# Performance work log

Hardware: AMD Instinct MI355X
Metric: run time of the kernel (lower is better)

## Reference

```python
import jax, jax.numpy as jnp
import numpy as np
from jax.scipy.special import logsumexp


def _lstm(x, mask, Wk, Wr, b, reverse=False):
    # x: [B,T,D], mask: [B,T] bool. Keras LSTM defaults: gate order i,f,g,o,
    # sigmoid recurrent activation, tanh activation. Masked steps carry state.
    if reverse:
        x = x[:, ::-1]
        mask = mask[:, ::-1]
    B, T, _ = x.shape
    H = Wr.shape[0]
    xz = jnp.einsum('btd,dh->bth', x, Wk) + b  # [B,T,4H] input projections, done once

    def step(carry, inp):
        h, c = carry
        z_t, m = inp  # [B,4H], [B]
        z = z_t + h @ Wr
        i, f, g, o = jnp.split(z, 4, axis=-1)
        i = jax.nn.sigmoid(i)
        f = jax.nn.sigmoid(f)
        g = jnp.tanh(g)
        o = jax.nn.sigmoid(o)
        c_new = f * c + i * g
        h_new = o * jnp.tanh(c_new)
        m = m[:, None]
        h = jnp.where(m, h_new, h)
        c = jnp.where(m, c_new, c)
        return (h, c), h

    h0 = jnp.zeros((B, H), x.dtype)
    (_, _), hs = jax.lax.scan(step, (h0, h0), (xz.transpose(1, 0, 2), mask.T))
    hs = hs.transpose(1, 0, 2)  # [B,T,H]
    if reverse:
        hs = hs[:, ::-1]
    return hs


def _crf_log_likelihood(logits, tags, lengths, trans):
    # TFA crf_log_likelihood: sequence_score - log_norm (forward algorithm)
    B, T, C = logits.shape
    t_idx = jnp.arange(T)
    mask = t_idx[None, :] < lengths[:, None]  # [B,T]
    # unary score: sum_t logits[b,t,tags[b,t]] over valid t
    unary = jnp.take_along_axis(logits, tags[..., None], axis=2)[..., 0]
    unary = jnp.sum(jnp.where(mask, unary, 0.0), axis=1)
    # binary score: sum_t trans[tags[t], tags[t+1]] for t < len-1
    binary = trans[tags[:, :-1], tags[:, 1:]]  # [B,T-1]
    mask2 = t_idx[None, : T - 1] < (lengths - 1)[:, None]
    binary = jnp.sum(jnp.where(mask2, binary, 0.0), axis=1)
    # log normalizer via forward algorithm scan
    alpha0 = logits[:, 0]  # [B,C]

    def step(alpha, inp):
        logit_t, m = inp  # [B,C], [B]
        new = logsumexp(alpha[:, :, None] + trans[None], axis=1) + logit_t
        alpha = jnp.where(m[:, None], new, alpha)
        return alpha, None

    alpha, _ = jax.lax.scan(step, alpha0,
                            (logits[:, 1:].transpose(1, 0, 2), mask[:, 1:].T))
    log_norm = logsumexp(alpha, axis=1)
    return unary + binary - log_norm


def setup_inputs() -> dict:
    key = jax.random.key(0)
    ks = jax.random.split(key, 12)
    V, D, H, C, B, T = 30000, 300, 256, 9, 64, 512
    lengths = jax.random.randint(ks[0], (B,), T // 4, T + 1).astype(jnp.int32)
    valid = jnp.arange(T)[None, :] < lengths[:, None]
    inputs = (jax.random.randint(ks[1], (B, T), 1, V) * valid).astype(jnp.int32)
    targets = (jax.random.randint(ks[2], (B, T), 0, C) * valid).astype(jnp.int32)
    s = 0.05
    return {
        'inputs': inputs,
        'inputs_length': lengths,
        'targets': targets,
        'embedding': jax.random.normal(ks[3], (V, D), jnp.float32) * s,
        'Wk_f': jax.random.normal(ks[4], (D, 4 * H), jnp.float32) * s,
        'Wr_f': jax.random.normal(ks[5], (H, 4 * H), jnp.float32) * s,
        'b_f': jnp.zeros((4 * H,), jnp.float32),
        'Wk_b': jax.random.normal(ks[6], (D, 4 * H), jnp.float32) * s,
        'Wr_b': jax.random.normal(ks[7], (H, 4 * H), jnp.float32) * s,
        'b_b': jnp.zeros((4 * H,), jnp.float32),
        'dense_W': jax.random.normal(ks[8], (2 * H, C), jnp.float32) * s,
        'dense_b': jnp.zeros((C,), jnp.float32),
        'trans': jax.random.uniform(ks[9], (C, C), jnp.float32),
    }


def reference(inputs, inputs_length, targets, embedding, Wk_f, Wr_f, b_f,
              Wk_b, Wr_b, b_b, dense_W, dense_b, trans):
    T = inputs.shape[1]
    mask = jnp.arange(T)[None, :] < inputs_length[:, None]  # [B,T]
    emb = embedding[inputs]  # [B,T,D] (dropout is identity in inference)
    h_f = _lstm(emb, mask, Wk_f, Wr_f, b_f, reverse=False)
    h_b = _lstm(emb, mask, Wk_b, Wr_b, b_b, reverse=True)
    h = jnp.concatenate([h_f, h_b], axis=-1)  # [B,T,2H]
    logits = h @ dense_W + dense_b  # [B,T,C]
    log_likelihood = _crf_log_likelihood(logits, targets, inputs_length, trans)
    return logits, log_likelihood, trans
```

## Files before the change

kernel.cpp:

```cpp
#include <hip/hip_runtime.h>
#include <cstdint>
#include <cstddef>

typedef unsigned int  u32;
typedef unsigned short u16;
typedef _Float16 f16;
typedef _Float16 f16x2 __attribute__((ext_vector_type(2)));
typedef _Float16 half8 __attribute__((ext_vector_type(8)));
typedef float    f32x4v __attribute__((ext_vector_type(4)));
typedef int      i32x4 __attribute__((ext_vector_type(4)));

#define BATCH 64
#define TSEQ  512
#define DEMB  300
#define KPAD  320
#define HDIM  256
#define G4    1024
#define NCLS  9

__device__ __forceinline__ u32 packf16(float a, float b) {
  f16x2 v; v.x = (f16)a; v.y = (f16)b;
  return __builtin_bit_cast(u32, v);
}
__device__ __forceinline__ float f16f(u16 x) {
  return (float)__builtin_bit_cast(f16, x);
}
__device__ __forceinline__ float sigm_fast(float x) {
  return __builtin_amdgcn_rcpf(1.f + __expf(-x));
}
__device__ __forceinline__ float tanh_fast(float x) {
  float ax = __builtin_fabsf(x);
  float e = __expf(-2.f * ax);
  float t = (1.f - e) * __builtin_amdgcn_rcpf(1.f + e);
  return copysignf(t, x);
}

__global__ __launch_bounds__(256) void embcvt_k(const float* __restrict__ emb,
                                                u16* __restrict__ out) {
  const int v  = blockIdx.x * 16 + (threadIdx.x >> 4);
  const int kc = threadIdx.x & 15;
  u32* __restrict__ dst = (u32*)(out + (size_t)v * KPAD + kc * 20);
  if (kc < 15) {
    const float* __restrict__ src = emb + (size_t)v * DEMB + kc * 20;
    float tmp[20];
#pragma unroll
    for (int j = 0; j < 20; ++j) tmp[j] = src[j];
#pragma unroll
    for (int j = 0; j < 10; ++j) dst[j] = packf16(tmp[2 * j], tmp[2 * j + 1]);
  } else {
#pragma unroll
    for (int j = 0; j < 10; ++j) dst[j] = 0u;
  }
}

__global__ __launch_bounds__(256) void wkt_k(const float* __restrict__ Wk_f,
                                             const float* __restrict__ Wk_b,
                                             u16* __restrict__ wkt) {
  const int dir = blockIdx.y;
  const float* __restrict__ Wk = dir ? Wk_b : Wk_f;
  const int col = blockIdx.x * 16 + (threadIdx.x >> 4);
  const int kc  = threadIdx.x & 15;
  u32* __restrict__ dst = (u32*)(wkt + ((size_t)dir * G4 + col) * KPAD + kc * 20);
  if (kc < 15) {
    float tmp[20];
#pragma unroll
    for (int j = 0; j < 20; ++j) tmp[j] = Wk[(size_t)(kc * 20 + j) * G4 + col];
#pragma unroll
    for (int j = 0; j < 10; ++j) dst[j] = packf16(tmp[2 * j], tmp[2 * j + 1]);
  } else {
#pragma unroll
    for (int j = 0; j < 10; ++j) dst[j] = 0u;
  }
}

__global__ __launch_bounds__(256) void wr8_k(const float* __restrict__ Wr_f,
                                             const float* __restrict__ Wr_b,
                                             signed char* __restrict__ wr8) {
  const int dir = blockIdx.y;
  const float* __restrict__ Wr = dir ? Wr_b : Wr_f;
  const int col = blockIdx.x * 16 + (threadIdx.x >> 4);
  const int k0  = (threadIdx.x & 15) * 16;
  float tmp[16];
#pragma unroll
  for (int j = 0; j < 16; ++j) tmp[j] = Wr[(size_t)(k0 + j) * G4 + col];
  u32 pw[4];
#pragma unroll
  for (int jj = 0; jj < 4; ++jj) {
    u32 p = 0;
#pragma unroll
    for (int b = 0; b < 4; ++b) {
      int q = (int)__builtin_rintf(tmp[4 * jj + b] * 512.f);
      q = q > 127 ? 127 : (q < -127 ? -127 : q);
      p |= ((u32)(q & 255)) << (8 * b);
    }
    pw[jj] = p;
  }
  *(uint4*)(wr8 + ((size_t)dir * G4 + col) * HDIM + k0) =
      make_uint4(pw[0], pw[1], pw[2], pw[3]);
}

__global__ __launch_bounds__(256) void xz_gemm_k(
    const int* __restrict__ inputs, const u16* __restrict__ wkt,
    const u16* __restrict__ embf16, const float* __restrict__ b_f,
    const float* __restrict__ b_b, u16* __restrict__ xz)
{
  __shared__ __align__(16) u16 As[128 * 40];
  __shared__ __align__(16) u16 Bs[128 * 40];
  const int tid  = threadIdx.x;
  const int wv   = tid >> 6, lane = tid & 63;
  const int quad = lane >> 4, fl = lane & 15;
  const int cbi  = blockIdx.x;
  const int dir  = cbi >> 3;
  const int cb1  = (cbi & 7) * 128;
  const int rb   = blockIdx.y * 128;
  const float* __restrict__ bias = dir ? b_b : b_f;

  const int sm = tid >> 1, sh = (tid & 1) * 16;
  const int vrow = inputs[rb + sm];
  const u16* __restrict__ asrc = wkt + ((size_t)(dir * G4) + cb1 + sm) * KPAD + sh;
  const u16* __restrict__ bsrc = embf16 + (size_t)vrow * KPAD + sh;

  f32x4v acc[2][8];
#pragma unroll
  for (int bt = 0; bt < 2; ++bt)
#pragma unroll
    for (int i = 0; i < 8; ++i) acc[bt][i] = (f32x4v){0.f, 0.f, 0.f, 0.f};

  for (int kt = 0; kt < 10; ++kt) {
    const int k0 = kt * 32;
    uint4 a0v = *(const uint4*)(asrc + k0);
    uint4 a1v = *(const uint4*)(asrc + k0 + 8);
    uint4 b0v = *(const uint4*)(bsrc + k0);
    uint4 b1v = *(const uint4*)(bsrc + k0 + 8);
    *(uint4*)&As[sm * 40 + sh]     = a0v;
    *(uint4*)&As[sm * 40 + sh + 8] = a1v;
    *(uint4*)&Bs[sm * 40 + sh]     = b0v;
    *(uint4*)&Bs[sm * 40 + sh + 8] = b1v;
    __syncthreads();
    half8 bf[2];
#pragma unroll
    for (int bt = 0; bt < 2; ++bt)
      bf[bt] = *(const half8*)&Bs[(wv * 32 + bt * 16 + fl) * 40 + quad * 8];
#pragma unroll
    for (int i = 0; i < 8; ++i) {
      half8 af = *(const half8*)&As[(i * 16 + fl) * 40 + quad * 8];
      acc[0][i] = __builtin_amdgcn_mfma_f32_16x16x32_f16(af, bf[0], acc[0][i], 0, 0, 0);
      acc[1][i] = __builtin_amdgcn_mfma_f32_16x16x32_f16(af, bf[1], acc[1][i], 0, 0, 0);
    }
    __syncthreads();
  }
#pragma unroll
  for (int bt = 0; bt < 2; ++bt) {
    const int row = rb + wv * 32 + bt * 16 + fl;
    u16* __restrict__ orow = xz + ((size_t)(dir * BATCH * TSEQ) + row) * G4;
#pragma unroll
    for (int i = 0; i < 8; ++i) {
      const int mb = cb1 + i * 16 + quad * 4;
      const float4 bb = *(const float4*)&bias[mb];
      f32x4v v = acc[bt][i];
      uint2 pk;
      pk.x = packf16(v[0] + bb.x, v[1] + bb.y);
      pk.y = packf16(v[2] + bb.z, v[3] + bb.w);
      *(uint2*)&orow[mb] = pk;
    }
  }
}

#define MFI(a, b, c) __builtin_amdgcn_mfma_i32_16x16x64_i8(a, b, c, 0, 0, 0)
#define LD8(t, kc) (*(const i32x4*)(wr8w + (size_t)(((t) >> 2) * 256 + 64 * w + ((t) & 3) * 16 + l15) * HDIM + (kc) * 64 + quad * 16))
#define DECL8(t) \
  i32x4 W##t##_0 = LD8(t, 0), W##t##_1 = LD8(t, 1), \
        W##t##_2 = LD8(t, 2), W##t##_3 = LD8(t, 3); \
  asm volatile("" : "+a"(W##t##_0), "+a"(W##t##_1), "+a"(W##t##_2), "+a"(W##t##_3));
#define TILE(t) \
  i32x4 ac##t = (i32x4){0, 0, 0, 0}; \
  ac##t = MFI(af0, W##t##_0, ac##t); ac##t = MFI(af1, W##t##_1, ac##t); \
  ac##t = MFI(af2, W##t##_2, ac##t); ac##t = MFI(af3, W##t##_3, ac##t);
#define SEL(a, b, c, d) \
  ((quad == 0) ? (a)[0] : (quad == 1) ? (b)[0] : (quad == 2) ? (c)[0] : (d)[0])

__global__ __launch_bounds__(256, 1) void lstm_k(
    const u16* __restrict__ xz, const signed char* __restrict__ wr8,
    const int* __restrict__ lengths, u16* __restrict__ hcat)
{
  const int chain = blockIdx.x;
  const int dir   = chain >> 6;
  const int batch = chain & 63;
  const int tid  = threadIdx.x;
  const int w    = tid >> 6;
  const int lane = tid & 63;
  const int quad = lane >> 4, l15 = lane & 15;
  const float DEQ = 1.f / (512.f * 127.f);

  __shared__ __align__(16) signed char hpk[2][256];

  const signed char* __restrict__ wr8w = wr8 + (size_t)dir * G4 * HDIM;

  DECL8(0)  DECL8(1)  DECL8(2)  DECL8(3)  DECL8(4)  DECL8(5)  DECL8(6)  DECL8(7)
  DECL8(8)  DECL8(9)  DECL8(10) DECL8(11) DECL8(12) DECL8(13) DECL8(14) DECL8(15)

  hpk[0][tid] = 0;

  float c = 0.f, h = 0.f;
  const int len = lengths[batch];
  const u16* __restrict__ xzb = xz + (size_t)(dir * BATCH + batch) * TSEQ * G4;
  u16* __restrict__ hrow = hcat + (size_t)batch * TSEQ * 512 + dir * 256;
  __syncthreads();

  int tt = dir ? (TSEQ - 1) : 0;
  const int dt = dir ? -1 : 1;
  u16 x0 = xzb[(size_t)tt * G4 + tid];
  u16 x1 = xzb[(size_t)tt * G4 + 256 + tid];
  u16 x2 = xzb[(size_t)tt * G4 + 512 + tid];
  u16 x3 = xzb[(size_t)tt * G4 + 768 + tid];

  for (int st = 0; st < TSEQ; ++st) {
    const int ttn = (st == TSEQ - 1) ? tt : tt + dt;
    u16 xn0 = xzb[(size_t)ttn * G4 + tid];
    u16 xn1 = xzb[(size_t)ttn * G4 + 256 + tid];
    u16 xn2 = xzb[(size_t)ttn * G4 + 512 + tid];
    u16 xn3 = xzb[(size_t)ttn * G4 + 768 + tid];

    const int par = st & 1;
    const signed char* hb = &hpk[par][0];
    i32x4 af0 = *(const i32x4*)(hb + quad * 16);
    i32x4 af1 = *(const i32x4*)(hb + 64 + quad * 16);
    i32x4 af2 = *(const i32x4*)(hb + 128 + quad * 16);
    i32x4 af3 = *(const i32x4*)(hb + 192 + quad * 16);

    TILE(0)  TILE(1)  TILE(2)  TILE(3)
    TILE(4)  TILE(5)  TILE(6)  TILE(7)
    TILE(8)  TILE(9)  TILE(10) TILE(11)
    TILE(12) TILE(13) TILE(14) TILE(15)

    int ri = SEL(ac0, ac1, ac2, ac3);
    int rf = SEL(ac4, ac5, ac6, ac7);
    int rg = SEL(ac8, ac9, ac10, ac11);
    int ro = SEL(ac12, ac13, ac14, ac15);

    float zi = (float)ri * DEQ + f16f(x0);
    float zf = (float)rf * DEQ + f16f(x1);
    float zg = (float)rg * DEQ + f16f(x2);
    float zo = (float)ro * DEQ + f16f(x3);
    float ig = sigm_fast(zi);
    float fg = sigm_fast(zf);
    float gg = tanh_fast(zg);
    float og = sigm_fast(zo);
    float cn = fg * c + ig * gg;
    float hn = og * tanh_fast(cn);
    if (tt < len) { c = cn; h = hn; }
    u32 hb2 = packf16(h, h);
    hrow[(size_t)tt * 512 + tid] = (u16)(hb2 & 0xffffu);
    int hq = (int)__builtin_rintf(h * 127.f);
    hpk[par ^ 1][tid] = (signed char)hq;
    __syncthreads();
    x0 = xn0; x1 = xn1; x2 = xn2; x3 = xn3; tt = ttn;
  }
}

__global__ __launch_bounds__(256) void dense_k(
    const u16* __restrict__ hcat, const float* __restrict__ W,
    const float* __restrict__ bias, float* __restrict__ out)
{
  const int lane = threadIdx.x & 63;
  const int wv = threadIdx.x >> 6;
  const int rowbase = (blockIdx.x * 4 + wv) * 8;
  for (int rr = 0; rr < 8; ++rr) {
    const int row = rowbase + rr;
    const u16* __restrict__ hr = hcat + (size_t)row * 512;
    float hv[8];
#pragma unroll
    for (int i = 0; i < 8; ++i)
      hv[i] = f16f(hr[i * 64 + lane]);
    float myout = 0.f;
#pragma unroll
    for (int cc = 0; cc < 9; ++cc) {
      float p = 0.f;
#pragma unroll
      for (int i = 0; i < 8; ++i)
        p = fmaf(hv[i], W[(size_t)(i * 64 + lane) * 9 + cc], p);
#pragma unroll
      for (int o = 32; o > 0; o >>= 1) p += __shfl_xor(p, o);
      if (lane == cc) myout = p + bias[cc];
    }
    if (lane < 9) out[(size_t)row * 9 + lane] = myout;
  }
}

__global__ __launch_bounds__(64) void crf_k(
    const float* __restrict__ logits, const int* __restrict__ tags,
    const int* __restrict__ lengths, const float* __restrict__ trans,
    float* __restrict__ out_ll, float* __restrict__ out_trans)
{
  const int b = blockIdx.x;
  const int lane = threadIdx.x;
  const int len = lengths[b];
  const float* __restrict__ lg = logits + (size_t)b * TSEQ * NCLS;
  const int* __restrict__ tg = tags + (size_t)b * TSEQ;

  float ua = 0.f, ba = 0.f;
  for (int t = lane; t < TSEQ; t += 64) {
    int tag = tg[t];
    if (t < len) ua += lg[t * 9 + tag];
    if (t < len - 1) ba += trans[tag * 9 + tg[t + 1]];
  }
  float s = ua + ba;
#pragma unroll
  for (int o = 32; o > 0; o >>= 1) s += __shfl_xor(s, o);

  const int j = (lane < 9) ? lane : 0;
  float trc[9], alpha[9];
#pragma unroll
  for (int i = 0; i < 9; ++i) trc[i] = trans[i * 9 + j];
#pragma unroll
  for (int i = 0; i < 9; ++i) alpha[i] = lg[i];
  for (int t = 1; t < TSEQ; ++t) {
    if (t >= len) break;
    float m = -1e30f;
#pragma unroll
    for (int i = 0; i < 9; ++i) m = fmaxf(m, alpha[i] + trc[i]);
    float ss = 0.f;
#pragma unroll
    for (int i = 0; i < 9; ++i) ss += __expf(alpha[i] + trc[i] - m);
    float nj = __logf(ss) + m + lg[t * 9 + j];
#pragma unroll
    for (int i = 0; i < 9; ++i) alpha[i] = __shfl(nj, i);
  }
  float m2 = -1e30f;
#pragma unroll
  for (int i = 0; i < 9; ++i) m2 = fmaxf(m2, alpha[i]);
  float s2 = 0.f;
#pragma unroll
  for (int i = 0; i < 9; ++i) s2 += __expf(alpha[i] - m2);
  float lse = __logf(s2) + m2;
  if (lane == 0) out_ll[b] = s - lse;
  if (b == 0)
    for (int i = lane; i < 81; i += 64) out_trans[i] = trans[i];
}

extern "C" void kernel_launch(void* const* d_in, const int* in_sizes, int n_in,
                              void* d_out, int out_size, void* d_ws, size_t ws_size,
                              hipStream_t stream)
{
  const int*   inputs  = (const int*)d_in[0];
  const int*   lengths = (const int*)d_in[1];
  const int*   targets = (const int*)d_in[2];
  const float* emb     = (const float*)d_in[3];
  const float* Wk_f    = (const float*)d_in[4];
  const float* Wr_f    = (const float*)d_in[5];
  const float* b_f     = (const float*)d_in[6];
  const float* Wk_b    = (const float*)d_in[7];
  const float* Wr_b    = (const float*)d_in[8];
  const float* b_b     = (const float*)d_in[9];
  const float* dense_W = (const float*)d_in[10];
  const float* dense_b = (const float*)d_in[11];
  const float* trans   = (const float*)d_in[12];

  char* ws = (char*)d_ws;
  u16*         wkt    = (u16*)ws;
  signed char* wr8    = (signed char*)(ws + 1310720ull);
  u16*         embf16 = (u16*)(ws + 1835008ull);
  u16*         xz     = (u16*)(ws + 1835008ull + 19200000ull);
  u16*         hcat   = (u16*)(ws + 1835008ull + 19200000ull + 134217728ull);

  float* out_logits = (float*)d_out;
  float* out_ll     = out_logits + (size_t)BATCH * TSEQ * NCLS;
  float* out_trans  = out_ll + BATCH;

  hipLaunchKernelGGL(embcvt_k, dim3(1875), dim3(256), 0, stream, emb, embf16);
  hipLaunchKernelGGL(wkt_k, dim3(64, 2), dim3(256), 0, stream, Wk_f, Wk_b, wkt);
  hipLaunchKernelGGL(wr8_k, dim3(64, 2), dim3(256), 0, stream, Wr_f, Wr_b, wr8);
  hipLaunchKernelGGL(xz_gemm_k, dim3(16, 256), dim3(256), 0, stream,
                     inputs, wkt, embf16, b_f, b_b, xz);
  hipLaunchKernelGGL(lstm_k, dim3(128), dim3(256), 0, stream,
                     xz, wr8, lengths, hcat);
  hipLaunchKernelGGL(dense_k, dim3(1024), dim3(256), 0, stream,
                     hcat, dense_W, dense_b, out_logits);
  hipLaunchKernelGGL(crf_k, dim3(64), dim3(64), 0, stream,
                     out_logits, targets, lengths, trans, out_ll, out_trans);
}
```

Measured before the change: 812.9 us.

## Split LSTM recurrent matvec across 8 waves to halve per-wave MFMA chain

The recurrent LSTM kernel now launches 512 threads (8 waves) per chain instead of 256. Each wave owns 32 hidden units and runs 8 MFMA tiles per step instead of 16, so it keeps half the register-resident int8 weights and has a shorter serial MFMA chain per timestep. Lanes in quads 0-1 hold the results and write h, while quads 2-3 compute redundant copies. The cost is more waves taking part in the per-step barrier, redundant gate math on half the lanes, and a launch bound of (512,2).

```diff
diff --git a/kernel.cpp b/kernel.cpp
--- a/kernel.cpp
+++ b/kernel.cpp
@@ -167,19 +167,20 @@
 }
 
 #define MFI(a, b, c) __builtin_amdgcn_mfma_i32_16x16x64_i8(a, b, c, 0, 0, 0)
-#define LD8(t, kc) (*(const i32x4*)(wr8w + (size_t)(((t) >> 2) * 256 + 64 * w + ((t) & 3) * 16 + l15) * HDIM + (kc) * 64 + quad * 16))
-#define DECL8(t) \
-  i32x4 W##t##_0 = LD8(t, 0), W##t##_1 = LD8(t, 1), \
-        W##t##_2 = LD8(t, 2), W##t##_3 = LD8(t, 3); \
-  asm volatile("" : "+a"(W##t##_0), "+a"(W##t##_1), "+a"(W##t##_2), "+a"(W##t##_3));
-#define TILE(t) \
-  i32x4 ac##t = (i32x4){0, 0, 0, 0}; \
-  ac##t = MFI(af0, W##t##_0, ac##t); ac##t = MFI(af1, W##t##_1, ac##t); \
-  ac##t = MFI(af2, W##t##_2, ac##t); ac##t = MFI(af3, W##t##_3, ac##t);
-#define SEL(a, b, c, d) \
-  ((quad == 0) ? (a)[0] : (quad == 1) ? (b)[0] : (quad == 2) ? (c)[0] : (d)[0])
-
-__global__ __launch_bounds__(256, 1) void lstm_k(
+#define LD8(g, ct, kc) (*(const i32x4*)(wr8w + (size_t)((g) * 256 + 32 * w + (ct) * 16 + l15) * HDIM + (kc) * 64 + q16))
+#define DECL8(g, ct) \
+  i32x4 W##g##ct##_0 = LD8(g, ct, 0), W##g##ct##_1 = LD8(g, ct, 1), \
+        W##g##ct##_2 = LD8(g, ct, 2), W##g##ct##_3 = LD8(g, ct, 3); \
+  asm volatile("" : "+a"(W##g##ct##_0), "+a"(W##g##ct##_1), \
+                    "+a"(W##g##ct##_2), "+a"(W##g##ct##_3));
+#define TILE(g, ct) \
+  i32x4 ac##g##ct = (i32x4){0, 0, 0, 0}; \
+  ac##g##ct = MFI(af0, W##g##ct##_0, ac##g##ct); \
+  ac##g##ct = MFI(af1, W##g##ct##_1, ac##g##ct); \
+  ac##g##ct = MFI(af2, W##g##ct##_2, ac##g##ct); \
+  ac##g##ct = MFI(af3, W##g##ct##_3, ac##g##ct);
+
+__global__ __launch_bounds__(512, 2) void lstm_k(
     const u16* __restrict__ xz, const signed char* __restrict__ wr8,
     const int* __restrict__ lengths, u16* __restrict__ hcat)
 {
@@ -190,16 +191,20 @@
   const int w    = tid >> 6;
   const int lane = tid & 63;
   const int quad = lane >> 4, l15 = lane & 15;
+  const int q16  = quad * 16;
+  const int ctsel = quad & 1;
+  const int j    = 32 * w + ctsel * 16 + l15;
+  const int wr   = quad < 2;
   const float DEQ = 1.f / (512.f * 127.f);
 
   __shared__ __align__(16) signed char hpk[2][256];
 
   const signed char* __restrict__ wr8w = wr8 + (size_t)dir * G4 * HDIM;
 
-  DECL8(0)  DECL8(1)  DECL8(2)  DECL8(3)  DECL8(4)  DECL8(5)  DECL8(6)  DECL8(7)
-  DECL8(8)  DECL8(9)  DECL8(10) DECL8(11) DECL8(12) DECL8(13) DECL8(14) DECL8(15)
-
-  hpk[0][tid] = 0;
+  DECL8(0, 0) DECL8(0, 1) DECL8(1, 0) DECL8(1, 1)
+  DECL8(2, 0) DECL8(2, 1) DECL8(3, 0) DECL8(3, 1)
+
+  if (tid < 256) hpk[0][tid] = 0;
 
   float c = 0.f, h = 0.f;
   const int len = lengths[batch];
@@ -209,34 +214,34 @@
 
   int tt = dir ? (TSEQ - 1) : 0;
   const int dt = dir ? -1 : 1;
-  u16 x0 = xzb[(size_t)tt * G4 + tid];
-  u16 x1 = xzb[(size_t)tt * G4 + 256 + tid];
-  u16 x2 = xzb[(size_t)tt * G4 + 512 + tid];
-  u16 x3 = xzb[(size_t)tt * G4 + 768 + tid];
+  u16 x0 = xzb[(size_t)tt * G4 + j];
+  u16 x1 = xzb[(size_t)tt * G4 + 256 + j];
+  u16 x2 = xzb[(size_t)tt * G4 + 512 + j];
+  u16 x3 = xzb[(size_t)tt * G4 + 768 + j];
 
   for (int st = 0; st < TSEQ; ++st) {
     const int ttn = (st == TSEQ - 1) ? tt : tt + dt;
-    u16 xn0 = xzb[(size_t)ttn * G4 + tid];
-    u16 xn1 = xzb[(size_t)ttn * G4 + 256 + tid];
-    u16 xn2 = xzb[(size_t)ttn * G4 + 512 + tid];
-    u16 xn3 = xzb[(size_t)ttn * G4 + 768 + tid];
+    u16 xn0 = xzb[(size_t)ttn * G4 + j];
+    u16 xn1 = xzb[(size_t)ttn * G4 + 256 + j];
+    u16 xn2 = xzb[(size_t)ttn * G4 + 512 + j];
+    u16 xn3 = xzb[(size_t)ttn * G4 + 768 + j];
 
     const int par = st & 1;
     const signed char* hb = &hpk[par][0];
-    i32x4 af0 = *(const i32x4*)(hb + quad * 16);
-    i32x4 af1 = *(const i32x4*)(hb + 64 + quad * 16);
-    i32x4 af2 = *(const i32x4*)(hb + 128 + quad * 16);
-    i32x4 af3 = *(const i32x4*)(hb + 192 + quad * 16);
-
-    TILE(0)  TILE(1)  TILE(2)  TILE(3)
-    TILE(4)  TILE(5)  TILE(6)  TILE(7)
-    TILE(8)  TILE(9)  TILE(10) TILE(11)
-    TILE(12) TILE(13) TILE(14) TILE(15)
-
-    int ri = SEL(ac0, ac1, ac2, ac3);
-    int rf = SEL(ac4, ac5, ac6, ac7);
-    int rg = SEL(ac8, ac9, ac10, ac11);
-    int ro = SEL(ac12, ac13, ac14, ac15);
+    i32x4 af0 = *(const i32x4*)(hb + q16);
+    i32x4 af1 = *(const i32x4*)(hb + 64 + q16);
+    i32x4 af2 = *(const i32x4*)(hb + 128 + q16);
+    i32x4 af3 = *(const i32x4*)(hb + 192 + q16);
+
+    TILE(0, 0) TILE(0, 1)
+    TILE(1, 0) TILE(1, 1)
+    TILE(2, 0) TILE(2, 1)
+    TILE(3, 0) TILE(3, 1)
+
+    int ri = ctsel ? ac01[0] : ac00[0];
+    int rf = ctsel ? ac11[0] : ac10[0];
+    int rg = ctsel ? ac21[0] : ac20[0];
+    int ro = ctsel ? ac31[0] : ac30[0];
 
     float zi = (float)ri * DEQ + f16f(x0);
     float zf = (float)rf * DEQ + f16f(x1);
@@ -249,10 +254,12 @@
     float cn = fg * c + ig * gg;
     float hn = og * tanh_fast(cn);
     if (tt < len) { c = cn; h = hn; }
-    u32 hb2 = packf16(h, h);
-    hrow[(size_t)tt * 512 + tid] = (u16)(hb2 & 0xffffu);
-    int hq = (int)__builtin_rintf(h * 127.f);
-    hpk[par ^ 1][tid] = (signed char)hq;
+    if (wr) {
+      u32 hb2 = packf16(h, h);
+      hrow[(size_t)tt * 512 + j] = (u16)(hb2 & 0xffffu);
+      int hq = (int)__builtin_rintf(h * 127.f);
+      hpk[par ^ 1][j] = (signed char)hq;
+    }
     __syncthreads();
     x0 = xn0; x1 = xn1; x2 = xn2; x3 = xn3; tt = ttn;
   }
@@ -372,7 +379,7 @@
   hipLaunchKernelGGL(wr8_k, dim3(64, 2), dim3(256), 0, stream, Wr_f, Wr_b, wr8);
   hipLaunchKernelGGL(xz_gemm_k, dim3(16, 256), dim3(256), 0, stream,
                      inputs, wkt, embf16, b_f, b_b, xz);
-  hipLaunchKernelGGL(lstm_k, dim3(128), dim3(256), 0, stream,
+  hipLaunchKernelGGL(lstm_k, dim3(128), dim3(512), 0, stream,
                      xz, wr8, lengths, hcat);
   hipLaunchKernelGGL(dense_k, dim3(1024), dim3(256), 0, stream,
                      hcat, dense_W, dense_b, out_logits);
```

New measurement: 718.9 us. 11.6% less time.
